# Kernel tuning notes

Measured on AMD Instinct MI355X. Metric: run time of the kernel, lower is better.

The kernel has to match this reference:

```python
import jax, jax.numpy as jnp
import numpy as np
from jax.scipy.special import logsumexp

# static problem sizes (all graphs identical size; pairs interleaved [q0,c0,q1,c1,...])
B = 64; NG = 2 * B; N = 48; E = 192; MAX_N = 64; MAX_E = 256
D_IN = 32; D = 128; EDGE_EMB = 128; M = 256; S = 64
T = 5; K = 3; TEMP = 0.1; SINK_ITERS = 10
VN = NG * N; VE = NG * E


def _mlp2(x, W1, b1, W2, b2):
    return jnp.maximum(x @ W1 + b1, 0.0) @ W2 + b2


def setup_inputs():
    keys = iter(jax.random.split(jax.random.key(0), 64))
    def w(fan_in, fan_out):
        return jax.random.normal(next(keys), (fan_in, fan_out), dtype=jnp.float32) * (1.0 / float(np.sqrt(fan_in)))
    z = lambda n: jnp.zeros((n,), jnp.float32)
    inp = {}
    inp['node_features'] = jax.random.normal(next(keys), (VN, D_IN), dtype=jnp.float32)
    inp['edge_features'] = jax.random.normal(next(keys), (VE, D_IN), dtype=jnp.float32)
    off = jnp.repeat(jnp.arange(NG, dtype=jnp.int32) * N, E)
    inp['from_idx'] = jax.random.randint(next(keys), (VE,), 0, N, dtype=jnp.int32) + off
    inp['to_idx'] = jax.random.randint(next(keys), (VE,), 0, N, dtype=jnp.int32) + off
    inp['enc_node_W'] = w(D_IN, D); inp['enc_node_b'] = z(D)
    inp['enc_edge_W'] = w(D_IN, EDGE_EMB); inp['enc_edge_b'] = z(EDGE_EMB)
    inp['ni_W1'] = w(2 * D, 2 * D); inp['ni_b1'] = z(2 * D)
    inp['ni_W2'] = w(2 * D, D); inp['ni_b2'] = z(D)
    ei_in = M + EDGE_EMB
    inp['ei_W1'] = w(ei_in, ei_in); inp['ei_b1'] = z(ei_in)
    inp['ei_W2'] = w(ei_in, EDGE_EMB); inp['ei_b2'] = z(EDGE_EMB)
    inp['msg_W'] = w(2 * D + EDGE_EMB, M); inp['msg_b'] = z(M)
    inp['nu_W1'] = w(D + M, 2 * D); inp['nu_b1'] = z(2 * D)
    inp['nu_W2'] = w(2 * D, D); inp['nu_b2'] = z(D)
    inp['ns_W1'] = w(D, S); inp['ns_b1'] = z(S)
    inp['ns_W2'] = w(S, S); inp['ns_b2'] = z(S)
    inp['es_W1'] = w(M, S); inp['es_b1'] = z(S)
    inp['es_W2'] = w(S, S); inp['es_b2'] = z(S)
    return inp


def _forward(node_features, edge_features, enc_node_W, enc_node_b, enc_edge_W, enc_edge_b,
             ni_W1, ni_b1, ni_W2, ni_b2, ei_W1, ei_b1, ei_W2, ei_b2, msg_W, msg_b,
             nu_W1, nu_b1, nu_W2, nu_b2, ns_W1, ns_b1, ns_W2, ns_b2,
             es_W1, es_b1, es_W2, es_b2, from_idx, to_idx):
    enc_n = node_features @ enc_node_W + enc_node_b            # [VN, D]
    enc_e = edge_features @ enc_edge_W + enc_edge_b            # [VE, EDGE_EMB]
    node_store = jnp.zeros((VN, D * (T + 1)), jnp.float32)
    edge_store = jnp.zeros((VE, M * (T + 1)), jnp.float32)
    # flat index of node/edge j of graph g inside interleaved padded store: g*max + j
    node_pad_idx = (jnp.arange(NG)[:, None] * MAX_N + jnp.arange(N)[None, :]).reshape(-1)
    edge_pad_idx = (jnp.arange(NG)[:, None] * MAX_E + jnp.arange(E)[None, :]).reshape(-1)
    node_mask = (jnp.arange(MAX_N) < N).astype(jnp.float32)[None, :, None]
    edge_mask = (jnp.arange(MAX_E) < E).astype(jnp.float32)[None, :, None]

    def transport(store, n_per, max_set, fdim, sW1, sb1, sW2, sb2, mask):
        x = store.reshape(NG, n_per, store.shape[-1])
        x = jnp.pad(x, ((0, 0), (0, max_set - n_per), (0, 0)))   # pad to max set size
        q, c = x[0::2], x[1::2]                                   # [B, max, dim_total]
        fq, fc = q[:, :, -fdim:], c[:, :, -fdim:]
        tq = _mlp2(fq, sW1, sb1, sW2, sb2) * mask
        tc = _mlp2(fc, sW1, sb1, sW2, sb2) * mask
        la = jnp.einsum('bqs,bcs->bqc', tq, tc) / TEMP
        for _ in range(SINK_ITERS):
            la = la - logsumexp(la, axis=2, keepdims=True)
            la = la - logsumexp(la, axis=1, keepdims=True)
        plan = jnp.exp(la)
        qi = jnp.einsum('bqc,bcd->bqd', plan, c)                  # query <- corpus
        ci = jnp.einsum('bqc,bqd->bcd', plan, q)                  # corpus <- query
        inter = jnp.stack([qi, ci], axis=1).reshape(NG * max_set, -1)
        return plan, inter, fq, fc

    for _ in range(K):  # time_update_steps
        h, e = enc_n, enc_e
        node_slots = [jnp.zeros((VN, D), jnp.float32)]
        edge_slots = [jnp.zeros((VE, M), jnp.float32)]
        for p in range(1, T + 1):  # propagation_steps
            h_comb = _mlp2(jnp.concatenate([h, node_store[:, (p - 1) * D:p * D]], -1), ni_W1, ni_b1, ni_W2, ni_b2)
            e_comb = _mlp2(jnp.concatenate([e, edge_store[:, (p - 1) * M:p * M]], -1), ei_W1, ei_b1, ei_W2, ei_b2)
            src, dst = h_comb[from_idx], h_comb[to_idx]
            fwd_msg = jnp.concatenate([src, dst, e_comb], -1) @ msg_W + msg_b
            bwd_msg = jnp.concatenate([dst, src, e_comb], -1) @ msg_W + msg_b
            agg = jax.ops.segment_sum(fwd_msg, to_idx, num_segments=VN) + jax.ops.segment_sum(bwd_msg, from_idx, num_segments=VN)
            h = _mlp2(jnp.concatenate([h_comb, agg], -1), nu_W1, nu_b1, nu_W2, nu_b2)
            src2, dst2 = h[from_idx], h[to_idx]
            msgs = (jnp.concatenate([src2, dst2, e_comb], -1) @ msg_W + msg_b) + \
                   (jnp.concatenate([dst2, src2, e_comb], -1) @ msg_W + msg_b)
            node_slots.append(h)
            edge_slots.append(msgs)
        upd_node = jnp.concatenate(node_slots, axis=1)
        upd_edge = jnp.concatenate(edge_slots, axis=1)
        n_plan, n_inter, ffq, ffc = transport(upd_node, N, MAX_N, D, ns_W1, ns_b1, ns_W2, ns_b2, node_mask)
        _, e_inter, _, _ = transport(upd_edge, E, MAX_E, M, es_W1, es_b1, es_W2, es_b2, edge_mask)
        node_store = jnp.concatenate([jnp.zeros((VN, D), jnp.float32), n_inter[node_pad_idx, D:]], axis=1)
        edge_store = jnp.concatenate([jnp.zeros((VE, M), jnp.float32), e_inter[edge_pad_idx, M:]], axis=1)

    # feature_alignment_score: -sum relu(q - P c)
    score = -jnp.sum(jnp.maximum(ffq - jnp.einsum('bqc,bcd->bqd', n_plan, ffc), 0.0), axis=(1, 2))
    return score


def reference(node_features, edge_features, from_idx, to_idx, enc_node_W, enc_node_b, enc_edge_W, enc_edge_b,
              ni_W1, ni_b1, ni_W2, ni_b2, ei_W1, ei_b1, ei_W2, ei_b2, msg_W, msg_b,
              nu_W1, nu_b1, nu_W2, nu_b2, ns_W1, ns_b1, ns_W2, ns_b2,
              es_W1, es_b1, es_W2, es_b2):
    return _forward(node_features, edge_features, enc_node_W, enc_node_b, enc_edge_W, enc_edge_b,
                    ni_W1, ni_b1, ni_W2, ni_b2, ei_W1, ei_b1, ei_W2, ei_b2, msg_W, msg_b,
                    nu_W1, nu_b1, nu_W2, nu_b2, ns_W1, ns_b1, ns_W2, ns_b2,
                    es_W1, es_b1, es_W2, es_b2, from_idx, to_idx)
```

## Files before the change

kernel.cpp:

```cpp
#include <hip/hip_runtime.h>
#include <cstdint>
#include <cstddef>

#define NGg   128
#define Bb    64
#define Nn    48
#define Ee    192
#define Sdim  64
#define VNn   6144
#define VEe   24576
#define INV_TEMP 10.0f
#define ADJ_STRIDE 96

typedef unsigned short u16;
typedef unsigned int   u32;
typedef __attribute__((ext_vector_type(8))) short short8;
typedef __attribute__((ext_vector_type(4))) float floatx4;

__device__ __forceinline__ u16 f2bf(float f)
{
    unsigned int u = __float_as_uint(f);
    u += 0x7FFFu + ((u >> 16) & 1u);
    return (u16)(u >> 16);
}
// ... 63 lines not shown
            #pragma unroll
            for (int q = 0; q < NB / 8; q++) {
                *(uint4*)&Bh[BR * TW + BKo + q * 8] = ((const uint4*)bh)[q];
                *(uint4*)&Bl[BR * TW + BKo + q * 8] = ((const uint4*)bl)[q];
            }
        }
        {
            const int kk = k0 + AKo;
            const u32* asrc = (kk < K1) ? A1 + (size_t)arow * lda1 + kk
                                        : A2 + (size_t)arow * lda2 + (kk - K1);
            u32 pk[NA];
            #pragma unroll
            for (int q = 0; q < NA / 4; q++)
                ((uint4*)pk)[q] = ((const uint4*)asrc)[q];
            u32 hi[NA / 2], lo[NA / 2];
            #pragma unroll
            for (int q = 0; q < NA / 2; q++) {
                hi[q] = __builtin_amdgcn_perm(pk[2 * q + 1], pk[2 * q], 0x05040100u);
                lo[q] = __builtin_amdgcn_perm(pk[2 * q + 1], pk[2 * q], 0x07060302u);
            }
            #pragma unroll
            for (int q = 0; q < NA / 8; q++) {
                *(uint4*)&Ah[AR * TW + AKo + q * 8] = ((uint4*)hi)[q];
                *(uint4*)&Al[AR * TW + AKo + q * 8] = ((uint4*)lo)[q];
            }
        }
        __syncthreads();
        short8 afh[FM], afl[FM], bfh[FN], bfl[FN];
        #pragma unroll
        for (int i = 0; i < FM; i++) {
            const int ro = (wm * (BM / 2) + i * 16 + l15) * TW + lq * 8;
            afh[i] = *(const short8*)&Ah[ro];
            afl[i] = *(const short8*)&Al[ro];
        }
        #pragma unroll
        for (int j = 0; j < FN; j++) {
            const int ro = (wn * (BN / 2) + j * 16 + l15) * TW + lq * 8;
            bfh[j] = *(const short8*)&Bh[ro];
            bfl[j] = *(const short8*)&Bl[ro];
        }
        #pragma unroll
        for (int i = 0; i < FM; i++)
            #pragma unroll
            for (int j = 0; j < FN; j++) {
                acc[i][j] = __builtin_amdgcn_mfma_f32_16x16x32_bf16(afh[i], bfl[j], acc[i][j], 0, 0, 0);
                acc[i][j] = __builtin_amdgcn_mfma_f32_16x16x32_bf16(afl[i], bfh[j], acc[i][j], 0, 0, 0);
                acc[i][j] = __builtin_amdgcn_mfma_f32_16x16x32_bf16(afh[i], bfh[j], acc[i][j], 0, 0, 0);
            }
        __syncthreads();
    }
    const int relu = flags & FL_RELU;
    const int opk  = flags & FL_OUTPK;
    #pragma unroll
    for (int j = 0; j < FN; j++) {
        const int col = bn + wn * (BN / 2) + j * 16 + l15;
        const bool cok = (col < Ncap);
        const float bv = (bias && cok) ? bias[col] : 0.f;
        #pragma unroll
        for (int i = 0; i < FM; i++) {
            const int row0 = bm + wm * (BM / 2) + i * 16 + lq * 4;
            #pragma unroll
            for (int r = 0; r < 4; r++) {
                float v = acc[i][j][r] + bv;
                if (relu) v = fmaxf(v, 0.f);
                if (cok) {
                    if (opk)
                        ((u32*)Cv)[(size_t)(row0 + r) * ldc + col] = packhl(v);
                    else
                        ((float*)Cv)[(size_t)(row0 + r) * ldc + col] = v;
                }
            }
        }
    }
}

static inline void gemmPK(hipStream_t s, int BM, int BN,
                          const u32* A1, int lda1, int K1,
                          const u32* A2, int lda2, int K2,
                          const u16* Wh, const u16* Wl, int ldwt,
                          const float* bias,
                          void* C, int ldc, int M, int Ngrid, int Ncap, int flags)
{
    dim3 grid(Ngrid / BN, M / BM);
    if (BM == 128 && BN == 128)
        gemm_pk_kernel<128, 128><<<grid, 256, 0, s>>>(A1, lda1, K1, A2, lda2, K2, Wh, Wl, ldwt, bias, C, ldc, Ncap, flags);
    else if (BM == 128 && BN == 64)
        gemm_pk_kernel<128, 64><<<grid, 256, 0, s>>>(A1, lda1, K1, A2, lda2, K2, Wh, Wl, ldwt, bias, C, ldc, Ncap, flags);
    else if (BM == 64 && BN == 128)
        gemm_pk_kernel<64, 128><<<grid, 256, 0, s>>>(A1, lda1, K1, A2, lda2, K2, Wh, Wl, ldwt, bias, C, ldc, Ncap, flags);
    else
        gemm_pk_kernel<64, 64><<<grid, 256, 0, s>>>(A1, lda1, K1, A2, lda2, K2, Wh, Wl, ldwt, bias, C, ldc, Ncap, flags);
}

struct GemmDesc {
    const u32* A1; int lda1, K1;
    const u32* A2; int lda2, K2;
    const u16* Wh; const u16* Wl; int ldwt;
    const float* bias;
    void* C; int ldc;
    int Ncap, flags, nx, nblk;
    const float* qs;
    const int* fidx; const int* tidx;
};

static inline GemmDesc mkDesc(const u32* A1, int lda1, int K1,
                              const u32* A2, int lda2, int K2,
                              const u16* Wh, const u16* Wl, int ldwt,
                              const float* bias, void* C, int ldc,
                              int M, int Ngrid, int Ncap, int flags)
{
    GemmDesc d;
    d.A1 = A1; d.lda1 = lda1; d.K1 = K1;
    d.A2 = A2; d.lda2 = lda2; d.K2 = K2;
    d.Wh = Wh; d.Wl = Wl; d.ldwt = ldwt;
    d.bias = bias; d.C = C; d.ldc = ldc;
    d.Ncap = Ncap; d.flags = flags;
    d.nx = Ngrid / 128; d.nblk = (M / 128) * (Ngrid / 128);
    d.qs = nullptr; d.fidx = nullptr; d.tidx = nullptr;
    return d;
}

__global__ __launch_bounds__(256) void gemm2_pk_kernel(GemmDesc d0, GemmDesc d1, int nb0)
{
    GemmDesc d;
    int local;
    if ((int)blockIdx.x < nb0) { d = d0; local = blockIdx.x; }
    else                       { d = d1; local = blockIdx.x - nb0; }
    const int by = local / d.nx, bx = local % d.nx;
    __shared__ __align__(16) u16 Ah[128 * TW];
    __shared__ __align__(16) u16 Al[128 * TW];
    __shared__ __align__(16) u16 Bh[128 * TW];
    __shared__ __align__(16) u16 Bl[128 * TW];
    const int tid = threadIdx.x;
    const int lane = tid & 63, wave = tid >> 6;
    const int wm = wave >> 1, wn = wave & 1;
    const int bm = by * 128, bn = bx * 128;
    const int K = d.K1 + d.K2;
    const int srow = tid >> 1;
    const int skoff = (tid & 1) * 16;
    const int arow = bm + srow;
    const int brow = bn + srow;
    const int l15 = lane & 15, lq = lane >> 4;

    floatx4 acc[4][4];
    #pragma unroll
    for (int i = 0; i < 4; i++)
        #pragma unroll
        for (int j = 0; j < 4; j++) acc[i][j] = (floatx4){0.f, 0.f, 0.f, 0.f};

    for (int k0 = 0; k0 < K; k0 += 32) {
        {
            const int kk = k0 + skoff;
            const u16* bh = d.Wh + (size_t)brow * d.ldwt + kk;
            const u16* bl = d.Wl + (size_t)brow * d.ldwt + kk;
            *(uint4*)&Bh[srow * TW + skoff]     = ((const uint4*)bh)[0];
            *(uint4*)&Bh[srow * TW + skoff + 8] = ((const uint4*)bh)[1];
            *(uint4*)&Bl[srow * TW + skoff]     = ((const uint4*)bl)[0];
            *(uint4*)&Bl[srow * TW + skoff + 8] = ((const uint4*)bl)[1];
        }
        {
            const int kk = k0 + skoff;
            const u32* asrc = (kk < d.K1) ? d.A1 + (size_t)arow * d.lda1 + kk
                                          : d.A2 + (size_t)arow * d.lda2 + (kk - d.K1);
            u32 pk[16];
            ((uint4*)pk)[0] = ((const uint4*)asrc)[0];
            ((uint4*)pk)[1] = ((const uint4*)asrc)[1];
            ((uint4*)pk)[2] = ((const uint4*)asrc)[2];
            ((uint4*)pk)[3] = ((const uint4*)asrc)[3];
            u32 hi[8], lo[8];
            #pragma unroll
            for (int q = 0; q < 8; q++) {
                hi[q] = __builtin_amdgcn_perm(pk[2 * q + 1], pk[2 * q], 0x05040100u);
                lo[q] = __builtin_amdgcn_perm(pk[2 * q + 1], pk[2 * q], 0x07060302u);
            }
            *(uint4*)&Ah[srow * TW + skoff]     = ((uint4*)hi)[0];
            *(uint4*)&Ah[srow * TW + skoff + 8] = ((uint4*)hi)[1];
            *(uint4*)&Al[srow * TW + skoff]     = ((uint4*)lo)[0];
            *(uint4*)&Al[srow * TW + skoff + 8] = ((uint4*)lo)[1];
        }
        __syncthreads();
        short8 afh[4], afl[4], bfh[4], bfl[4];
        #pragma unroll
        for (int i = 0; i < 4; i++) {
            const int ro = (wm * 64 + i * 16 + l15) * TW + lq * 8;
            afh[i] = *(const short8*)&Ah[ro];
            afl[i] = *(const short8*)&Al[ro];
        }
        #pragma unroll
        for (int j = 0; j < 4; j++) {
            const int ro = (wn * 64 + j * 16 + l15) * TW + lq * 8;
            bfh[j] = *(const short8*)&Bh[ro];
            bfl[j] = *(const short8*)&Bl[ro];
        }
        #pragma unroll
        for (int i = 0; i < 4; i++)
            #pragma unroll
            for (int j = 0; j < 4; j++) {
                acc[i][j] = __builtin_amdgcn_mfma_f32_16x16x32_bf16(afh[i], bfl[j], acc[i][j], 0, 0, 0);
                acc[i][j] = __builtin_amdgcn_mfma_f32_16x16x32_bf16(afl[i], bfh[j], acc[i][j], 0, 0, 0);
                acc[i][j] = __builtin_amdgcn_mfma_f32_16x16x32_bf16(afh[i], bfh[j], acc[i][j], 0, 0, 0);
            }
        __syncthreads();
    }
    if (d.flags & FL_MSGS) {
        #pragma unroll
        for (int i = 0; i < 4; i++) {
            #pragma unroll
            for (int r = 0; r < 4; r++) {
                const int row = bm + wm * 64 + i * 16 + lq * 4 + r;
                const int fi = d.fidx[row], ti = d.tidx[row];
                #pragma unroll
                for (int j = 0; j < 4; j++) {
                    const int col = bn + wn * 64 + j * 16 + l15;
                    float v = 2.f * (acc[i][j][r] + d.bias[col])
                            + d.qs[(size_t)fi * 256 + col] + d.qs[(size_t)ti * 256 + col];
                    ((u32*)d.C)[(size_t)row * d.ldc + col] = packhl(v);
                }
            }
        }
        return;
    }
    const int relu = d.flags & FL_RELU;
    const int opk  = d.flags & FL_OUTPK;
    #pragma unroll
    for (int j = 0; j < 4; j++) {
        const int col = bn + wn * 64 + j * 16 + l15;
        const bool cok = (col < d.Ncap);
        const float bv = (d.bias && cok) ? d.bias[col] : 0.f;
        #pragma unroll
        for (int i = 0; i < 4; i++) {
            const int row0 = bm + wm * 64 + i * 16 + lq * 4;
            #pragma unroll
            for (int r = 0; r < 4; r++) {
                float v = acc[i][j][r] + bv;
                if (relu) v = fmaxf(v, 0.f);
                if (cok) {
                    if (opk)
                        ((u32*)d.C)[(size_t)(row0 + r) * d.ldc + col] = packhl(v);
                    else
                        ((float*)d.C)[(size_t)(row0 + r) * d.ldc + col] = v;
                }
            }
        }
    }
}

static inline void gemm2(hipStream_t s, const GemmDesc& d0, const GemmDesc& d1)
{
    gemm2_pk_kernel<<<d0.nblk + d1.nblk, 256, 0, s>>>(d0, d1, d0.nblk);
}
static inline void gemm1(hipStream_t s, const GemmDesc& d0)
{
    gemm2_pk_kernel<<<d0.nblk, 256, 0, s>>>(d0, d0, d0.nblk);
}

__global__ __launch_bounds__(256) void gemm_es1msgs_kernel(
    const u32* __restrict__ A,
    const float* __restrict__ qs,
    const int* __restrict__ fidx, const int* __restrict__ tidx,
    const u16* __restrict__ Wh, const u16* __restrict__ Wl,
    const float* __restrict__ bias,
    u32* __restrict__ C)
{
    __shared__ __align__(16) u16 Ah[128 * TW];
    __shared__ __align__(16) u16 Al[128 * TW];
    __shared__ __align__(16) u16 Bh[64 * TW];
    __shared__ __align__(16) u16 Bl[64 * TW];
    const int tid = threadIdx.x;
    const int lane = tid & 63, wave = tid >> 6;
    const int wm = wave >> 1, wn = wave & 1;
    const int bm = blockIdx.y * 128;
    const int AR = tid >> 1, AKo = (tid & 1) * 16;
    const int BR = tid >> 2, BKo = (tid & 3) * 8;
    const int arow = bm + AR;
    const int l15 = lane & 15, lq = lane >> 4;
    const int fi = fidx[arow], ti = tidx[arow];

    floatx4 acc[4][2];
    #pragma unroll
    for (int i = 0; i < 4; i++)
        #pragma unroll
        for (int j = 0; j < 2; j++) acc[i][j] = (floatx4){0.f, 0.f, 0.f, 0.f};

    for (int k0 = 0; k0 < 256; k0 += 32) {
        {
            const int kk = k0 + BKo;
            const u16* bh = Wh + (size_t)BR * 256 + kk;
            const u16* bl = Wl + (size_t)BR * 256 + kk;
            *(uint4*)&Bh[BR * TW + BKo] = ((const uint4*)bh)[0];
            *(uint4*)&Bl[BR * TW + BKo] = ((const uint4*)bl)[0];
        }
        {
            const int kk = k0 + AKo;
            const u32* asrc = A + (size_t)arow * 256 + kk;
            u32 pk[16];
            ((uint4*)pk)[0] = ((const uint4*)asrc)[0];
            ((uint4*)pk)[1] = ((const uint4*)asrc)[1];
            ((uint4*)pk)[2] = ((const uint4*)asrc)[2];
            ((uint4*)pk)[3] = ((const uint4*)asrc)[3];
            float qf[16], qt[16];
            const float* qfp = qs + (size_t)fi * 256 + kk;
            const float* qtp = qs + (size_t)ti * 256 + kk;
            #pragma unroll
            for (int q = 0; q < 4; q++) {
                ((float4*)qf)[q] = ((const float4*)qfp)[q];
                ((float4*)qt)[q] = ((const float4*)qtp)[q];
            }
            u16 ph[16], pl8[16];
            #pragma unroll
            for (int q = 0; q < 16; q++) {
                float v = qf[q] + qt[q] + 2.f * unpackhl(pk[q]);
                u16 h = f2bf(v);
                ph[q] = h;
                pl8[q] = f2bf(v - bf2f(h));
            }
            *(uint4*)&Ah[AR * TW + AKo]     = *(const uint4*)&ph[0];
            *(uint4*)&Ah[AR * TW + AKo + 8] = *(const uint4*)&ph[8];
            *(uint4*)&Al[AR * TW + AKo]     = *(const uint4*)&pl8[0];
            *(uint4*)&Al[AR * TW + AKo + 8] = *(const uint4*)&pl8[8];
        }
        __syncthreads();
        short8 afh[4], afl[4], bfh[2], bfl[2];
        #pragma unroll
        for (int i = 0; i < 4; i++) {
            const int ro = (wm * 64 + i * 16 + l15) * TW + lq * 8;
            afh[i] = *(const short8*)&Ah[ro];
            afl[i] = *(const short8*)&Al[ro];
        }
        #pragma unroll
        for (int j = 0; j < 2; j++) {
            const int ro = (wn * 32 + j * 16 + l15) * TW + lq * 8;
            bfh[j] = *(const short8*)&Bh[ro];
            bfl[j] = *(const short8*)&Bl[ro];
        }
        #pragma unroll
        for (int i = 0; i < 4; i++)
// ... 546 lines not shown
#define OFF_ENC_N      47972352ULL
#define OFF_ENC_E      48758784ULL
#define OFF_N_LA       51904512ULL
#define OFF_WT         52199424ULL
#define OFF_WTL        52547584ULL
#define OFF_ARENA      52895744ULL
#define OFF_DEG        66265088ULL
#define OFF_ADJ        66271232ULL
#define TOTAL_FLOATS   66861056ULL

#define WT_NIW1   0
#define WT_NIW2   65536
#define WT_EIW1   98304
#define WT_EIW2   245760
#define WT_MSG    294912
#define WT_P01    393216
#define WT_NUW1   458752
#define WT_NUW2   557056
#define WT_WSUM   589824
#define WT_ENCN   622592
#define WT_ENCE   626688
#define WT_NS1    630784
#define WT_NS2    647168
#define WT_ES1    655360
#define WT_ES2    688128

#define PK(p) ((u32*)(p))

extern "C" void kernel_launch(void* const* d_in, const int* in_sizes, int n_in,
                              void* d_out, int out_size, void* d_ws, size_t ws_size,
                              hipStream_t stream)
{
    (void)in_sizes; (void)n_in; (void)out_size;
    if (ws_size < TOTAL_FLOATS * sizeof(float)) {
        diag_kernel<<<1, 64, 0, stream>>>((float*)d_out, (float)ws_size);
        return;
    }

    const float* node_features = (const float*)d_in[0];
    const float* edge_features = (const float*)d_in[1];
    const int*   from_idx      = (const int*)d_in[2];
    const int*   to_idx        = (const int*)d_in[3];
    const float* enc_node_W = (const float*)d_in[4];
    const float* enc_node_b = (const float*)d_in[5];
    const float* enc_edge_W = (const float*)d_in[6];
    const float* enc_edge_b = (const float*)d_in[7];
    const float* ni_W1 = (const float*)d_in[8];
    const float* ni_b1 = (const float*)d_in[9];
    const float* ni_W2 = (const float*)d_in[10];
    const float* ni_b2 = (const float*)d_in[11];
    const float* ei_W1 = (const float*)d_in[12];
    const float* ei_b1 = (const float*)d_in[13];
    const float* ei_W2 = (const float*)d_in[14];
    const float* ei_b2 = (const float*)d_in[15];
    const float* msg_W = (const float*)d_in[16];
    const float* msg_b = (const float*)d_in[17];
    const float* nu_W1 = (const float*)d_in[18];
    const float* nu_b1 = (const float*)d_in[19];
    const float* nu_W2 = (const float*)d_in[20];
    const float* nu_b2 = (const float*)d_in[21];
    const float* ns_W1 = (const float*)d_in[22];
    const float* ns_b1 = (const float*)d_in[23];
    const float* ns_W2 = (const float*)d_in[24];
    const float* ns_b2 = (const float*)d_in[25];
    const float* es_W1 = (const float*)d_in[26];
    const float* es_b1 = (const float*)d_in[27];
    const float* es_W2 = (const float*)d_in[28];
    const float* es_b2 = (const float*)d_in[29];

    float* ws = (float*)d_ws;
    float* upd_node   = ws + OFF_UPD_NODE;
    float* node_store = ws + OFF_NODE_STORE;
    float* edge_store = ws + OFF_EDGE_STORE;
    float* ecomb      = ws + OFF_ECOMB;
    float* enc_n      = ws + OFF_ENC_N;
    float* enc_e      = ws + OFF_ENC_E;
    float* n_la       = ws + OFF_N_LA;
    u16* WT  = (u16*)(ws + OFF_WT);
    u16* WTL = (u16*)(ws + OFF_WTL);
    float* arena      = ws + OFF_ARENA;
    int* deg = (int*)(ws + OFF_DEG);
    u32* adj = (u32*)(ws + OFF_ADJ);

    float* A_hidden = arena;
    float* A_hcomb  = arena + 1572864;
    float* A_ehid   = arena + 2359296;
    float* A_ec2    = arena + 2359296;
    float* A_P01    = arena + 8650752;
    float* A_aggb   = arena + 11796480;
    float* B_Qs       = arena;
    float* B_Qs2      = ecomb + (size_t)4 * VEe * 128;
    float* B_thid_e   = arena + 8650752;
    float* B_ttreal_e = arena + 10223616;
    float* B_ela      = arena + 2359296;
    float* B_msgs     = arena + 6553600;
    float* B_thid_n   = arena + 12058624;
    float* B_ttreal_n = arena + 12451840;

    prep_kernel<<<(696320 + 255) / 256, 256, 0, stream>>>(
        ni_W1, ni_W2, ei_W1, ei_W2, msg_W, nu_W1, nu_W2,
        enc_node_W, enc_edge_W, ns_W1, ns_W2, es_W1, es_W2, WT, WTL);
    zero_deg_kernel<<<VNn / 256, 256, 0, stream>>>(deg);
    csr_build_kernel<<<VEe / 256, 256, 0, stream>>>(from_idx, to_idx, deg, adj);

    gemm_f32_kernel<<<dim3(1, VNn / 128), 256, 0, stream>>>(
        node_features, 32, 32, WT + WT_ENCN, WTL + WT_ENCN, 32, enc_node_b, PK(enc_n), 128, 128);
    gemm_f32_kernel<<<dim3(1, VEe / 128), 256, 0, stream>>>(
        edge_features, 32, 32, WT + WT_ENCE, WTL + WT_ENCE, 32, enc_edge_b, PK(enc_e), 128, 128);

    for (int k = 0; k < 3; k++) {
        for (int p = 1; p <= 5; p++) {
            const bool hs = (k > 0) && (p > 1);
            const u32* hA1 = (p == 1) ? PK(enc_n) : PK(upd_node + (size_t)(p - 2) * 128);
            const int  hlda1 = (p == 1) ? 128 : 640;
            const u32* hA2 = hs ? PK(node_store + (size_t)(p - 2) * 128) : nullptr;
            const int  hK2 = hs ? 128 : 0;
            GemmDesc hcomb1_d = mkDesc(hA1, hlda1, 128, hA2, 512, hK2,
                                       WT + WT_NIW1, WTL + WT_NIW1, 256, ni_b1,
                                       A_hidden, 256, VNn, 256, 256, FL_RELU | FL_OUTPK);
            GemmDesc hcomb2_d = mkDesc(PK(A_hidden), 256, 256, nullptr, 0, 0,
                                       WT + WT_NIW2, WTL + WT_NIW2, 256, ni_b2,
                                       A_hcomb, 128, VNn, 128, 128, FL_OUTPK);
            GemmDesc p01_d = mkDesc(PK(A_hcomb), 128, 128, nullptr, 0, 0,
                                    WT + WT_P01, WTL + WT_P01, 128, nullptr,
                                    A_P01, 512, VNn, 512, 512, FL_OUTPK);

            const bool edge_full = ((k == 0 && p == 1) || (k > 0 && p > 1));
            if (edge_full) {
                const u32* esrc = (k == 0) ? nullptr : PK(edge_store + (size_t)(p - 2) * 256);
                const int  eK2  = (k == 0) ? 0 : 256;
                float* ec_slot = (k == 0) ? ecomb : ecomb + (size_t)(p - 1) * VEe * 128;
                GemmDesc eiW1_d = mkDesc(PK(enc_e), 128, 128, esrc, 1024, eK2,
                                         WT + WT_EIW1, WTL + WT_EIW1, 384, ei_b1,
                                         A_ehid, 384, VEe, 384, 384, FL_RELU | FL_OUTPK);
                GemmDesc eiW2_d = mkDesc(PK(A_ehid), 384, 384, nullptr, 0, 0,
                                         WT + WT_EIW2, WTL + WT_EIW2, 384, ei_b2,
                                         ec_slot, 128, VEe, 128, 128, FL_OUTPK);
                GemmDesc ec2_d = mkDesc(PK(ec_slot), 128, 128, nullptr, 0, 0,
                                        WT + WT_MSG + 256, WTL + WT_MSG + 256, 384, msg_b,
                                        A_ec2, 256, VEe, 256, 256, FL_OUTPK);
                gemm2(stream, eiW1_d, hcomb1_d);
                gemm2(stream, eiW2_d, hcomb2_d);
                gemm2(stream, ec2_d, p01_d);
            } else if (k > 0 && p == 1) {
                GemmDesc ec2_d = mkDesc(PK(ecomb), 128, 128, nullptr, 0, 0,
                                        WT + WT_MSG + 256, WTL + WT_MSG + 256, 384, msg_b,
                                        A_ec2, 256, VEe, 256, 256, FL_OUTPK);
                gemm2(stream, ec2_d, hcomb1_d);
                gemmPK(stream, 64, 64, PK(A_hidden), 256, 256, nullptr, 0, 0,
                       WT + WT_NIW2, WTL + WT_NIW2, 256,
                       ni_b2, A_hcomb, 128, VNn, 128, 128, FL_OUTPK);
                gemmPK(stream, 64, 128, PK(A_hcomb), 128, 128, nullptr, 0, 0,
                       WT + WT_P01, WTL + WT_P01, 128,
                       nullptr, A_P01, 512, VNn, 512, 512, FL_OUTPK);
            } else {
                gemmPK(stream, 64, 64, hA1, hlda1, 128, hA2, 512, hK2,
                       WT + WT_NIW1, WTL + WT_NIW1, 256, ni_b1,
                       A_hidden, 256, VNn, 256, 256, FL_RELU | FL_OUTPK);
                gemmPK(stream, 64, 64, PK(A_hidden), 256, 256, nullptr, 0, 0,
                       WT + WT_NIW2, WTL + WT_NIW2, 256,
                       ni_b2, A_hcomb, 128, VNn, 128, 128, FL_OUTPK);
                gemmPK(stream, 64, 128, PK(A_hcomb), 128, 128, nullptr, 0, 0,
                       WT + WT_P01, WTL + WT_P01, 128,
                       nullptr, A_P01, 512, VNn, 512, 512, FL_OUTPK);
            }
            agg_csr_kernel<<<VNn, 256, 0, stream>>>(PK(A_P01), PK(A_ec2), deg, adj, PK(A_aggb));
            gemmPK(stream, 64, 64, PK(A_hcomb), 128, 128, PK(A_aggb), 256, 256,
                   WT + WT_NUW1, WTL + WT_NUW1, 384,
                   nu_b1, A_hidden, 256, VNn, 256, 256, FL_RELU | FL_OUTPK);
            gemmPK(stream, 64, 64, PK(A_hidden), 256, 256, nullptr, 0, 0,
                   WT + WT_NUW2, WTL + WT_NUW2, 256,
                   nu_b2, upd_node + (size_t)(p - 1) * 128, 640, VNn, 128, 128, FL_OUTPK);
        }
        if (k < 2) {
            GemmDesc qs_d = mkDesc(PK(upd_node + 512), 640, 128, nullptr, 0, 0,
                                   WT + WT_WSUM, WTL + WT_WSUM, 128, nullptr,
                                   B_Qs, 256, VNn, 256, 256, 0);
            GemmDesc ns1_d = mkDesc(PK(upd_node + 512), 640, 128, nullptr, 0, 0,
                                    WT + WT_NS1, WTL + WT_NS1, 128, ns_b1,
                                    B_thid_n, 64, VNn, 128, 64, FL_RELU | FL_OUTPK);
            gemm2(stream, qs_d, ns1_d);
            gemm_es1msgs_kernel<<<dim3(1, VEe / 128), 256, 0, stream>>>(
                PK(A_ec2), B_Qs, from_idx, to_idx,
                WT + WT_ES1, WTL + WT_ES1, es_b1, PK(B_thid_e));
            GemmDesc es2_d = mkDesc(PK(B_thid_e), 64, 64, nullptr, 0, 0,
                                    WT + WT_ES2, WTL + WT_ES2, 64, es_b2,
                                    B_ttreal_e, 64, VEe, 128, 64, 0);
            GemmDesc ns2_d = mkDesc(PK(B_thid_n), 64, 64, nullptr, 0, 0,
                                    WT + WT_NS2, WTL + WT_NS2, 64, ns_b2,
                                    B_ttreal_n, 64, VNn, 128, 64, 0);
            gemm2(stream, es2_d, ns2_d);
            la_fused_kernel<<<64 + 1024, 256, 0, stream>>>(B_ttreal_n, PK(n_la), B_ttreal_e, B_ela);
            sinkhorn256_kernel<<<Bb, 1024, 0, stream>>>(B_ela);
            bgemmDual(stream, PK(n_la), 64, 48, PK(upd_node), 640, PK(node_store), 512, 512);
            float* qsbuf[2] = { B_Qs2, B_Qs };
            GemmDesc qs1_d = mkDesc(PK(upd_node), 640, 128, nullptr, 0, 0,
                                    WT + WT_WSUM, WTL + WT_WSUM, 128, nullptr,
                                    qsbuf[0], 256, VNn, 256, 256, 0);
            gemm1(stream, qs1_d);
            for (int sl = 1; sl <= 4; sl++) {
                const size_t ss = (k == 0) ? 0 : (size_t)(sl - 1);
                GemmDesc em_d = mkDesc(PK(ecomb + ss * VEe * 128), 128, 128, nullptr, 0, 0,
                                       WT + WT_MSG + 256, WTL + WT_MSG + 256, 384, msg_b,
                                       B_msgs, 256, VEe, 256, 256, FL_MSGS);
                em_d.qs = qsbuf[(sl - 1) & 1];
                em_d.fidx = from_idx; em_d.tidx = to_idx;
                if (sl < 4) {
                    GemmDesc qsn_d = mkDesc(PK(upd_node + (size_t)sl * 128), 640, 128,
                                            nullptr, 0, 0,
                                            WT + WT_WSUM, WTL + WT_WSUM, 128, nullptr,
                                            qsbuf[sl & 1], 256, VNn, 256, 256, 0);
                    gemm2(stream, em_d, qsn_d);
                } else {
                    gemm1(stream, em_d);
                }
                bgemmDual(stream, PK(B_ela), 256, 192, PK(B_msgs), 256,
                          PK(edge_store + (size_t)(sl - 1) * 256), 1024, 256);
            }
        } else {
            gemmPK(stream, 64, 64, PK(upd_node + 512), 640, 128, nullptr, 0, 0,
                   WT + WT_NS1, WTL + WT_NS1, 128,
                   ns_b1, B_thid_n, 64, VNn, 64, 64, FL_RELU | FL_OUTPK);
            gemmPK(stream, 64, 64, PK(B_thid_n), 64, 64, nullptr, 0, 0,
                   WT + WT_NS2, WTL + WT_NS2, 64,
                   ns_b2, B_ttreal_n, 64, VNn, 64, 64, 0);
            la_fused_kernel<<<64, 256, 0, stream>>>(B_ttreal_n, PK(n_la), B_ttreal_e, B_ela);
        }
    }
    score_kernel<<<Bb, 128, 0, stream>>>(PK(upd_node), PK(n_la), (float*)d_out);
}
```

Baseline: 2.794 ms.

## Fuse node two-layer MLPs into one kernel and reschedule edge GEMMs alongside

Adds an mlp2_kernel that computes both layers of the node-side MLPs (node interaction and node update) per 64-row block, keeping the relu hidden layer in shared memory instead of writing it to global memory and launching a second GEMM. The same launch can also carry a 128x128 edge-side GEMM tile set in its leading blocks, so edge encoder work overlaps with node MLPs. The per-step loop is re-sequenced so the next step's edge GEMMs are paired with the current node-update MLP. This cuts launches and the hidden-activation round trip, but each node block recomputes with a large B1 tile (256 columns), uses heavy shared memory and registers, and the gemmPK dispatcher loses its 128x64 and 64x128 variants.

```diff
diff --git a/kernel.cpp b/kernel.cpp
--- a/kernel.cpp
+++ b/kernel.cpp
@@ -169,14 +169,10 @@
                           void* C, int ldc, int M, int Ngrid, int Ncap, int flags)
 {
     dim3 grid(Ngrid / BN, M / BM);
-    if (BM == 128 && BN == 128)
+    if (BM == 64 && BN == 64)
+        gemm_pk_kernel<64, 64><<<grid, 256, 0, s>>>(A1, lda1, K1, A2, lda2, K2, Wh, Wl, ldwt, bias, C, ldc, Ncap, flags);
+    else
         gemm_pk_kernel<128, 128><<<grid, 256, 0, s>>>(A1, lda1, K1, A2, lda2, K2, Wh, Wl, ldwt, bias, C, ldc, Ncap, flags);
-    else if (BM == 128 && BN == 64)
-        gemm_pk_kernel<128, 64><<<grid, 256, 0, s>>>(A1, lda1, K1, A2, lda2, K2, Wh, Wl, ldwt, bias, C, ldc, Ncap, flags);
-    else if (BM == 64 && BN == 128)
-        gemm_pk_kernel<64, 128><<<grid, 256, 0, s>>>(A1, lda1, K1, A2, lda2, K2, Wh, Wl, ldwt, bias, C, ldc, Ncap, flags);
-    else
-        gemm_pk_kernel<64, 64><<<grid, 256, 0, s>>>(A1, lda1, K1, A2, lda2, K2, Wh, Wl, ldwt, bias, C, ldc, Ncap, flags);
 }
 
 struct GemmDesc {
@@ -339,6 +335,283 @@
 static inline void gemm1(hipStream_t s, const GemmDesc& d0)
 {
     gemm2_pk_kernel<<<d0.nblk, 256, 0, s>>>(d0, d0, d0.nblk);
+}
+
+struct MlpDesc {
+    const u32* A1; int lda1, K1;
+    const u32* A2; int lda2, K2;
+    const u16* W1h; const u16* W1l; int ldw1;
+    const float* b1;
+    const u16* W2h; const u16* W2l;
+    const float* b2;
+    u32* C; int ldc;
+};
+
+#define HSTR 44
+
+__global__ __launch_bounds__(256) void mlp2_kernel(GemmDesc e, int nbE, MlpDesc m)
+{
+    __shared__ __align__(16) u16 S[25600];
+    const int tid = threadIdx.x;
+    const int lane = tid & 63, wave = tid >> 6;
+    const int wm = wave >> 1, wn = wave & 1;
+    const int l15 = lane & 15, lq = lane >> 4;
+
+    if ((int)blockIdx.x < nbE) {
+        u16* Ah = S;
+        u16* Al = S + 5120;
+        u16* Bh = S + 10240;
+        u16* Bl = S + 15360;
+        const int local = blockIdx.x;
+        const int by = local / e.nx, bx = local % e.nx;
+        const int bm = by * 128, bn = bx * 128;
+        const int K = e.K1 + e.K2;
+        const int srow = tid >> 1;
+        const int skoff = (tid & 1) * 16;
+        const int arow = bm + srow;
+        const int brow = bn + srow;
+
+        floatx4 acc[4][4];
+        #pragma unroll
+        for (int i = 0; i < 4; i++)
+            #pragma unroll
+            for (int j = 0; j < 4; j++) acc[i][j] = (floatx4){0.f, 0.f, 0.f, 0.f};
+
+        for (int k0 = 0; k0 < K; k0 += 32) {
+            {
+                const int kk = k0 + skoff;
+                const u16* bh = e.Wh + (size_t)brow * e.ldwt + kk;
+                const u16* bl = e.Wl + (size_t)brow * e.ldwt + kk;
+                *(uint4*)&Bh[srow * TW + skoff]     = ((const uint4*)bh)[0];
+                *(uint4*)&Bh[srow * TW + skoff + 8] = ((const uint4*)bh)[1];
+                *(uint4*)&Bl[srow * TW + skoff]     = ((const uint4*)bl)[0];
+                *(uint4*)&Bl[srow * TW + skoff + 8] = ((const uint4*)bl)[1];
+            }
+            {
+                const int kk = k0 + skoff;
+                const u32* asrc = (kk < e.K1) ? e.A1 + (size_t)arow * e.lda1 + kk
+                                              : e.A2 + (size_t)arow * e.lda2 + (kk - e.K1);
+                u32 pk[16];
+                ((uint4*)pk)[0] = ((const uint4*)asrc)[0];
+                ((uint4*)pk)[1] = ((const uint4*)asrc)[1];
+                ((uint4*)pk)[2] = ((const uint4*)asrc)[2];
+                ((uint4*)pk)[3] = ((const uint4*)asrc)[3];
+                u32 hi[8], lo[8];
+                #pragma unroll
+                for (int q = 0; q < 8; q++) {
+                    hi[q] = __builtin_amdgcn_perm(pk[2 * q + 1], pk[2 * q], 0x05040100u);
+                    lo[q] = __builtin_amdgcn_perm(pk[2 * q + 1], pk[2 * q], 0x07060302u);
+                }
+                *(uint4*)&Ah[srow * TW + skoff]     = ((uint4*)hi)[0];
+                *(uint4*)&Ah[srow * TW + skoff + 8] = ((uint4*)hi)[1];
+                *(uint4*)&Al[srow * TW + skoff]     = ((uint4*)lo)[0];
+                *(uint4*)&Al[srow * TW + skoff + 8] = ((uint4*)lo)[1];
+            }
+            __syncthreads();
+            short8 afh[4], afl[4], bfh[4], bfl[4];
+            #pragma unroll
+            for (int i = 0; i < 4; i++) {
+                const int ro = (wm * 64 + i * 16 + l15) * TW + lq * 8;
+                afh[i] = *(const short8*)&Ah[ro];
+                afl[i] = *(const short8*)&Al[ro];
+            }
+            #pragma unroll
+            for (int j = 0; j < 4; j++) {
+                const int ro = (wn * 64 + j * 16 + l15) * TW + lq * 8;
+                bfh[j] = *(const short8*)&Bh[ro];
+                bfl[j] = *(const short8*)&Bl[ro];
+            }
+            #pragma unroll
+            for (int i = 0; i < 4; i++)
+                #pragma unroll
+                for (int j = 0; j < 4; j++) {
+                    acc[i][j] = __builtin_amdgcn_mfma_f32_16x16x32_bf16(afh[i], bfl[j], acc[i][j], 0, 0, 0);
+                    acc[i][j] = __builtin_amdgcn_mfma_f32_16x16x32_bf16(afl[i], bfh[j], acc[i][j], 0, 0, 0);
+                    acc[i][j] = __builtin_amdgcn_mfma_f32_16x16x32_bf16(afh[i], bfh[j], acc[i][j], 0, 0, 0);
+                }
+            __syncthreads();
+        }
+        const int relu = e.flags & FL_RELU;
+        #pragma unroll
+        for (int j = 0; j < 4; j++) {
+            const int col = bn + wn * 64 + j * 16 + l15;
+            const float bv = e.bias ? e.bias[col] : 0.f;
+            #pragma unroll
+            for (int i = 0; i < 4; i++) {
+                const int row0 = bm + wm * 64 + i * 16 + lq * 4;
+                #pragma unroll
+                for (int r = 0; r < 4; r++) {
+                    float v = acc[i][j][r] + bv;
+                    if (relu) v = fmaxf(v, 0.f);
+                    ((u32*)e.C)[(size_t)(row0 + r) * e.ldc + col] = packhl(v);
+                }
+            }
+        }
+        return;
+    }
+    const int brow = (blockIdx.x - nbE) * 64;
+    u16* A1h = S;
+    u16* A1l = S + 2560;
+    u16* B1h = S + 5120;
+    u16* B1l = S + 15360;
+    const int K = m.K1 + m.K2;
+    const int AR = tid >> 2, AKo = (tid & 3) * 8;
+    const int arow = brow + AR;
+
+    floatx4 acc1[2][8];
+    #pragma unroll
+    for (int i = 0; i < 2; i++)
+        #pragma unroll
+        for (int j = 0; j < 8; j++) acc1[i][j] = (floatx4){0.f, 0.f, 0.f, 0.f};
+
+    for (int k0 = 0; k0 < K; k0 += 32) {
+        {
+            const int kk = k0 + AKo;
+            const u32* asrc = (kk < m.K1) ? m.A1 + (size_t)arow * m.lda1 + kk
+                                          : m.A2 + (size_t)arow * m.lda2 + (kk - m.K1);
+            u32 pk[8];
+            ((uint4*)pk)[0] = ((const uint4*)asrc)[0];
+            ((uint4*)pk)[1] = ((const uint4*)asrc)[1];
+            u32 hi[4], lo[4];
+            #pragma unroll
+            for (int q = 0; q < 4; q++) {
+                hi[q] = __builtin_amdgcn_perm(pk[2 * q + 1], pk[2 * q], 0x05040100u);
+                lo[q] = __builtin_amdgcn_perm(pk[2 * q + 1], pk[2 * q], 0x07060302u);
+            }
+            *(uint4*)&A1h[AR * TW + AKo] = *(uint4*)hi;
+            *(uint4*)&A1l[AR * TW + AKo] = *(uint4*)lo;
+        }
+        {
+            const u16* bh = m.W1h + (size_t)tid * m.ldw1 + k0;
+            const u16* bl = m.W1l + (size_t)tid * m.ldw1 + k0;
+            #pragma unroll
+            for (int q = 0; q < 4; q++) {
+                *(uint4*)&B1h[tid * TW + q * 8] = ((const uint4*)bh)[q];
+                *(uint4*)&B1l[tid * TW + q * 8] = ((const uint4*)bl)[q];
+            }
+        }
+        __syncthreads();
+        short8 afh[2], afl[2];
+        #pragma unroll
+        for (int i = 0; i < 2; i++) {
+            const int ro = (wm * 32 + i * 16 + l15) * TW + lq * 8;
+            afh[i] = *(const short8*)&A1h[ro];
+            afl[i] = *(const short8*)&A1l[ro];
+        }
+        #pragma unroll
+        for (int jh = 0; jh < 2; jh++) {
+            short8 bfh[4], bfl[4];
+            #pragma unroll
+            for (int jj = 0; jj < 4; jj++) {
+                const int col = wn * 128 + (jh * 4 + jj) * 16 + l15;
+                const int ro = col * TW + lq * 8;
+                bfh[jj] = *(const short8*)&B1h[ro];
+                bfl[jj] = *(const short8*)&B1l[ro];
+            }
+            #pragma unroll
+            for (int i = 0; i < 2; i++)
+                #pragma unroll
+                for (int jj = 0; jj < 4; jj++) {
+                    const int j = jh * 4 + jj;
+                    acc1[i][j] = __builtin_amdgcn_mfma_f32_16x16x32_bf16(afh[i], bfl[jj], acc1[i][j], 0, 0, 0);
+                    acc1[i][j] = __builtin_amdgcn_mfma_f32_16x16x32_bf16(afl[i], bfh[jj], acc1[i][j], 0, 0, 0);
+                    acc1[i][j] = __builtin_amdgcn_mfma_f32_16x16x32_bf16(afh[i], bfh[jj], acc1[i][j], 0, 0, 0);
+                }
+        }
+        __syncthreads();
+    }
+    u32* Hc  = (u32*)S;
+    u16* B2h = S + 5632;
+    u16* B2l = S + 10752;
+    floatx4 acc2[2][4];
+    #pragma unroll
+    for (int i = 0; i < 2; i++)
+        #pragma unroll
+        for (int j = 0; j < 4; j++) acc2[i][j] = (floatx4){0.f, 0.f, 0.f, 0.f};
+
+    for (int kt = 0; kt < 8; kt++) {
+        const int wn0 = kt >> 2, j0 = (kt & 3) * 2;
+        if (wn == wn0) {
+            #pragma unroll
+            for (int i = 0; i < 2; i++)
+                #pragma unroll
+                for (int jj = 0; jj < 2; jj++) {
+                    const int j = j0 + jj;
+                    const int colg = wn0 * 128 + j * 16 + l15;
+                    const float bv = m.b1[colg];
+                    #pragma unroll
+                    for (int r = 0; r < 4; r++) {
+                        const int row = wm * 32 + i * 16 + lq * 4 + r;
+                        Hc[row * HSTR + jj * 16 + l15] = packhl(fmaxf(acc1[i][j][r] + bv, 0.f));
+                    }
+                }
+        }
+        {
+            const int r2 = tid >> 1, ko2 = (tid & 1) * 16;
+            const u16* w2h = m.W2h + (size_t)r2 * 256 + kt * 32 + ko2;
+            const u16* w2l = m.W2l + (size_t)r2 * 256 + kt * 32 + ko2;
+            *(uint4*)&B2h[r2 * TW + ko2]     = ((const uint4*)w2h)[0];
+            *(uint4*)&B2h[r2 * TW + ko2 + 8] = ((const uint4*)w2h)[1];
+            *(uint4*)&B2l[r2 * TW + ko2]     = ((const uint4*)w2l)[0];
+            *(uint4*)&B2l[r2 * TW + ko2 + 8] = ((const uint4*)w2l)[1];
+        }
+        __syncthreads();
+        short8 afh[2], afl[2];
+        #pragma unroll
+        for (int i = 0; i < 2; i++) {
+            const int row = wm * 32 + i * 16 + l15;
+            u32 w[8];
+            *(uint4*)&w[0] = *(const uint4*)&Hc[row * HSTR + lq * 8];
+            *(uint4*)&w[4] = *(const uint4*)&Hc[row * HSTR + lq * 8 + 4];
+            u32 hi[4], lo[4];
+            #pragma unroll
+            for (int q = 0; q < 4; q++) {
+                hi[q] = __builtin_amdgcn_perm(w[2 * q + 1], w[2 * q], 0x05040100u);
+                lo[q] = __builtin_amdgcn_perm(w[2 * q + 1], w[2 * q], 0x07060302u);
+            }
+            afh[i] = *(short8*)hi;
+            afl[i] = *(short8*)lo;
+        }
+        short8 bfh[4], bfl[4];
+        #pragma unroll
+        for (int j = 0; j < 4; j++) {
+            const int col = wn * 64 + j * 16 + l15;
+            const int ro = col * TW + lq * 8;
+            bfh[j] = *(const short8*)&B2h[ro];
+            bfl[j] = *(const short8*)&B2l[ro];
+        }
+        #pragma unroll
+        for (int i = 0; i < 2; i++)
+            #pragma unroll
+            for (int j = 0; j < 4; j++) {
+                acc2[i][j] = __builtin_amdgcn_mfma_f32_16x16x32_bf16(afh[i], bfl[j], acc2[i][j], 0, 0, 0);
+                acc2[i][j] = __builtin_amdgcn_mfma_f32_16x16x32_bf16(afl[i], bfh[j], acc2[i][j], 0, 0, 0);
+                acc2[i][j] = __builtin_amdgcn_mfma_f32_16x16x32_bf16(afh[i], bfh[j], acc2[i][j], 0, 0, 0);
+            }
+        __syncthreads();
+    }
+    #pragma unroll
+    for (int j = 0; j < 4; j++) {
+        const int colg = wn * 64 + j * 16 + l15;
+        const float bv = m.b2[colg];
+        #pragma unroll
+        for (int i = 0; i < 2; i++) {
+            const int row0 = brow + wm * 32 + i * 16 + lq * 4;
+            #pragma unroll
+            for (int r = 0; r < 4; r++)
+                m.C[(size_t)(row0 + r) * m.ldc + colg] = packhl(acc2[i][j][r] + bv);
+        }
+    }
+}
+
+static inline void mlpE(hipStream_t s, const GemmDesc& e, const MlpDesc& m)
+{
+    mlp2_kernel<<<e.nblk + VNn / 64, 256, 0, s>>>(e, e.nblk, m);
+}
+static inline void mlp0(hipStream_t s, const MlpDesc& m)
+{
+    GemmDesc dummy = {};
+    mlp2_kernel<<<VNn / 64, 256, 0, s>>>(dummy, 0, m);
 }
 
 __global__ __launch_bounds__(256) void gemm_es1msgs_kernel(
@@ -1051,7 +1324,6 @@
     int* deg = (int*)(ws + OFF_DEG);
     u32* adj = (u32*)(ws + OFF_ADJ);
 
-    float* A_hidden = arena;
     float* A_hcomb  = arena + 1572864;
     float* A_ehid   = arena + 2359296;
     float* A_ec2    = arena + 2359296;
@@ -1077,69 +1349,81 @@
     gemm_f32_kernel<<<dim3(1, VEe / 128), 256, 0, stream>>>(
         edge_features, 32, 32, WT + WT_ENCE, WTL + WT_ENCE, 32, enc_edge_b, PK(enc_e), 128, 128);
 
+    auto mkHC = [&](int k, int p) {
+        MlpDesc d;
+        d.A1 = (p == 1) ? PK(enc_n) : PK(upd_node + (size_t)(p - 2) * 128);
+        d.lda1 = (p == 1) ? 128 : 640; d.K1 = 128;
+        const bool hs = (k > 0) && (p > 1);
+        d.A2 = hs ? PK(node_store + (size_t)(p - 2) * 128) : nullptr;
+        d.lda2 = 512; d.K2 = hs ? 128 : 0;
+        d.W1h = WT + WT_NIW1; d.W1l = WTL + WT_NIW1; d.ldw1 = 256; d.b1 = ni_b1;
+        d.W2h = WT + WT_NIW2; d.W2l = WTL + WT_NIW2; d.b2 = ni_b2;
+        d.C = PK(A_hcomb); d.ldc = 128;
+        return d;
+    };
+    auto mkNU = [&](int p) {
+        MlpDesc d;
+        d.A1 = PK(A_hcomb); d.lda1 = 128; d.K1 = 128;
+        d.A2 = PK(A_aggb);  d.lda2 = 256; d.K2 = 256;
+        d.W1h = WT + WT_NUW1; d.W1l = WTL + WT_NUW1; d.ldw1 = 384; d.b1 = nu_b1;
+        d.W2h = WT + WT_NUW2; d.W2l = WTL + WT_NUW2; d.b2 = nu_b2;
+        d.C = PK(upd_node + (size_t)(p - 1) * 128); d.ldc = 640;
+        return d;
+    };
+    auto mkE1 = [&](int k, int p) {
+        const bool st = (k > 0) && (p > 1);
+        return mkDesc(PK(enc_e), 128, 128,
+                      st ? PK(edge_store + (size_t)(p - 2) * 256) : nullptr, 1024, st ? 256 : 0,
+                      WT + WT_EIW1, WTL + WT_EIW1, 384, ei_b1,
+                      A_ehid, 384, VEe, 384, 384, FL_RELU | FL_OUTPK);
+    };
+    auto mkE2 = [&](int p) {
+        return mkDesc(PK(A_ehid), 384, 384, nullptr, 0, 0,
+                      WT + WT_EIW2, WTL + WT_EIW2, 384, ei_b2,
+                      ecomb + (size_t)(p - 1) * VEe * 128, 128, VEe, 128, 128, FL_OUTPK);
+    };
+    auto mkE3 = [&](int slot) {
+        return mkDesc(PK(ecomb + (size_t)slot * VEe * 128), 128, 128, nullptr, 0, 0,
+                      WT + WT_MSG + 256, WTL + WT_MSG + 256, 384, msg_b,
+                      A_ec2, 256, VEe, 256, 256, FL_OUTPK);
+    };
+    auto mkP01 = [&]() {
+        return mkDesc(PK(A_hcomb), 128, 128, nullptr, 0, 0,
+                      WT + WT_P01, WTL + WT_P01, 128, nullptr,
+                      A_P01, 512, VNn, 512, 512, FL_OUTPK);
+    };
+    auto doAgg = [&]() {
+        agg_csr_kernel<<<VNn, 256, 0, stream>>>(PK(A_P01), PK(A_ec2), deg, adj, PK(A_aggb));
+    };
+
     for (int k = 0; k < 3; k++) {
-        for (int p = 1; p <= 5; p++) {
-            const bool hs = (k > 0) && (p > 1);
-            const u32* hA1 = (p == 1) ? PK(enc_n) : PK(upd_node + (size_t)(p - 2) * 128);
-            const int  hlda1 = (p == 1) ? 128 : 640;
-            const u32* hA2 = hs ? PK(node_store + (size_t)(p - 2) * 128) : nullptr;
-            const int  hK2 = hs ? 128 : 0;
-            GemmDesc hcomb1_d = mkDesc(hA1, hlda1, 128, hA2, 512, hK2,
-                                       WT + WT_NIW1, WTL + WT_NIW1, 256, ni_b1,
-                                       A_hidden, 256, VNn, 256, 256, FL_RELU | FL_OUTPK);
-            GemmDesc hcomb2_d = mkDesc(PK(A_hidden), 256, 256, nullptr, 0, 0,
-                                       WT + WT_NIW2, WTL + WT_NIW2, 256, ni_b2,
-                                       A_hcomb, 128, VNn, 128, 128, FL_OUTPK);
-            GemmDesc p01_d = mkDesc(PK(A_hcomb), 128, 128, nullptr, 0, 0,
-                                    WT + WT_P01, WTL + WT_P01, 128, nullptr,
-                                    A_P01, 512, VNn, 512, 512, FL_OUTPK);
-
-            const bool edge_full = ((k == 0 && p == 1) || (k > 0 && p > 1));
-            if (edge_full) {
-                const u32* esrc = (k == 0) ? nullptr : PK(edge_store + (size_t)(p - 2) * 256);
-                const int  eK2  = (k == 0) ? 0 : 256;
-                float* ec_slot = (k == 0) ? ecomb : ecomb + (size_t)(p - 1) * VEe * 128;
-                GemmDesc eiW1_d = mkDesc(PK(enc_e), 128, 128, esrc, 1024, eK2,
-                                         WT + WT_EIW1, WTL + WT_EIW1, 384, ei_b1,
-                                         A_ehid, 384, VEe, 384, 384, FL_RELU | FL_OUTPK);
-                GemmDesc eiW2_d = mkDesc(PK(A_ehid), 384, 384, nullptr, 0, 0,
-                                         WT + WT_EIW2, WTL + WT_EIW2, 384, ei_b2,
-                                         ec_slot, 128, VEe, 128, 128, FL_OUTPK);
-                GemmDesc ec2_d = mkDesc(PK(ec_slot), 128, 128, nullptr, 0, 0,
-                                        WT + WT_MSG + 256, WTL + WT_MSG + 256, 384, msg_b,
-                                        A_ec2, 256, VEe, 256, 256, FL_OUTPK);
-                gemm2(stream, eiW1_d, hcomb1_d);
-                gemm2(stream, eiW2_d, hcomb2_d);
-                gemm2(stream, ec2_d, p01_d);
-            } else if (k > 0 && p == 1) {
-                GemmDesc ec2_d = mkDesc(PK(ecomb), 128, 128, nullptr, 0, 0,
-                                        WT + WT_MSG + 256, WTL + WT_MSG + 256, 384, msg_b,
-                                        A_ec2, 256, VEe, 256, 256, FL_OUTPK);
-                gemm2(stream, ec2_d, hcomb1_d);
-                gemmPK(stream, 64, 64, PK(A_hidden), 256, 256, nullptr, 0, 0,
-                       WT + WT_NIW2, WTL + WT_NIW2, 256,
-                       ni_b2, A_hcomb, 128, VNn, 128, 128, FL_OUTPK);
-                gemmPK(stream, 64, 128, PK(A_hcomb), 128, 128, nullptr, 0, 0,
-                       WT + WT_P01, WTL + WT_P01, 128,
-                       nullptr, A_P01, 512, VNn, 512, 512, FL_OUTPK);
-            } else {
-                gemmPK(stream, 64, 64, hA1, hlda1, 128, hA2, 512, hK2,
-                       WT + WT_NIW1, WTL + WT_NIW1, 256, ni_b1,
-                       A_hidden, 256, VNn, 256, 256, FL_RELU | FL_OUTPK);
-                gemmPK(stream, 64, 64, PK(A_hidden), 256, 256, nullptr, 0, 0,
-                       WT + WT_NIW2, WTL + WT_NIW2, 256,
-                       ni_b2, A_hcomb, 128, VNn, 128, 128, FL_OUTPK);
-                gemmPK(stream, 64, 128, PK(A_hcomb), 128, 128, nullptr, 0, 0,
-                       WT + WT_P01, WTL + WT_P01, 128,
-                       nullptr, A_P01, 512, VNn, 512, 512, FL_OUTPK);
-            }
-            agg_csr_kernel<<<VNn, 256, 0, stream>>>(PK(A_P01), PK(A_ec2), deg, adj, PK(A_aggb));
-            gemmPK(stream, 64, 64, PK(A_hcomb), 128, 128, PK(A_aggb), 256, 256,
-                   WT + WT_NUW1, WTL + WT_NUW1, 384,
-                   nu_b1, A_hidden, 256, VNn, 256, 256, FL_RELU | FL_OUTPK);
-            gemmPK(stream, 64, 64, PK(A_hidden), 256, 256, nullptr, 0, 0,
-                   WT + WT_NUW2, WTL + WT_NUW2, 256,
-                   nu_b2, upd_node + (size_t)(p - 1) * 128, 640, VNn, 128, 128, FL_OUTPK);
+        if (k == 0) {
+            mlpE(stream, mkE1(0, 1), mkHC(0, 1));
+            gemm1(stream, mkE2(1));
+            gemm2(stream, mkE3(0), mkP01());
+            doAgg();
+            mlp0(stream, mkNU(1));
+            for (int p = 2; p <= 5; p++) {
+                mlp0(stream, mkHC(0, p));
+                gemm1(stream, mkP01());
+                doAgg();
+                mlp0(stream, mkNU(p));
+            }
+        } else {
+            mlpE(stream, mkE3(0), mkHC(k, 1));
+            gemm1(stream, mkP01());
+            doAgg();
+            mlpE(stream, mkE1(k, 2), mkNU(1));
+            mlpE(stream, mkE2(2), mkHC(k, 2));
+            for (int p = 2; p <= 4; p++) {
+                gemm2(stream, mkE3(p - 1), mkP01());
+                doAgg();
+                mlpE(stream, mkE1(k, p + 1), mkNU(p));
+                mlpE(stream, mkE2(p + 1), mkHC(k, p + 1));
+            }
+            gemm2(stream, mkE3(4), mkP01());
+            doAgg();
+            mlp0(stream, mkNU(5));
         }
         if (k < 2) {
             GemmDesc qs_d = mkDesc(PK(upd_node + 512), 640, 128, nullptr, 0, 0,
```

Measured after the change: 3.623 ms. 29.7% more time.
